# Optimization experiments

Hardware: AMD Instinct MI355X
Metric: run time of the kernel (lower is better)

The kernel has to match this reference:

```python
import jax, jax.numpy as jnp
import numpy as np

B, L, H, D, N, R, K = 1, 2048, 2048, 4096, 16, 128, 4


def setup_inputs() -> dict:
    key = jax.random.key(0)
    ks = jax.random.split(key, 10)
    s = 0.02
    x = jax.random.normal(ks[0], (B, L, H), dtype=jnp.float32)
    W_in = jax.random.normal(ks[1], (H, 2 * D), dtype=jnp.float32) * s
    conv_w = jax.random.normal(ks[2], (K, D), dtype=jnp.float32) * s  # depthwise causal conv
    conv_b = jnp.zeros((D,), dtype=jnp.float32)
    W_x = jax.random.normal(ks[3], (D, R + 2 * N), dtype=jnp.float32) * s
    W_dt = jax.random.normal(ks[4], (R, D), dtype=jnp.float32) * (R ** -0.5)
    # dt bias initialized so softplus(b_dt) ~ dt in [1e-3, 1e-1]
    dt = jnp.exp(jax.random.uniform(ks[5], (D,)) * (np.log(0.1) - np.log(1e-3)) + np.log(1e-3))
    b_dt = dt + jnp.log(-jnp.expm1(-dt))
    A_log = jnp.broadcast_to(jnp.log(jnp.arange(1, N + 1, dtype=jnp.float32)), (D, N))
    D_param = jnp.ones((D,), dtype=jnp.float32)
    W_out = jax.random.normal(ks[6], (D, H), dtype=jnp.float32) * s
    return {"x": x, "W_in": W_in, "conv_w": conv_w, "conv_b": conv_b,
            "W_x": W_x, "W_dt": W_dt, "b_dt": b_dt, "A_log": A_log,
            "D_param": D_param, "W_out": W_out}


def _mamba_fwd(x, W_in, conv_w, conv_b, W_x, W_dt, b_dt, A_log, D_param, W_out):
    silu = jax.nn.silu
    # in_proj then chunk into hidden / gate: [B,L,D] each
    proj = x @ W_in
    hs, gate = jnp.split(proj, 2, axis=-1)
    # causal depthwise conv along sequence (pad K-1 on the left)
    hs_pad = jnp.pad(hs, ((0, 0), (K - 1, 0), (0, 0)))
    conv = sum(hs_pad[:, k:k + L, :] * conv_w[k] for k in range(K)) + conv_b
    hs = silu(conv)  # [B,L,D]
    # ssm parameters
    ssm_p = hs @ W_x  # [B,L,R+2N]
    dt_in, Bm, Cm = jnp.split(ssm_p, [R, R + N], axis=-1)
    dt = jax.nn.softplus(dt_in @ W_dt + b_dt)  # [B,L,D]
    A = -jnp.exp(A_log)  # [D,N]
    dA = jnp.exp(dt[..., None] * A)                       # [B,L,D,N]
    dBu = dt[..., None] * Bm[:, :, None, :] * hs[..., None]  # [B,L,D,N]

    def step(s, inp):
        dA_t, dBu_t, C_t = inp
        s = dA_t * s + dBu_t                 # [B,D,N]
        y = jnp.einsum('bdn,bn->bd', s, C_t)
        return s, y

    s0 = jnp.zeros((B, D, N), dtype=x.dtype)
    xs = (jnp.moveaxis(dA, 1, 0), jnp.moveaxis(dBu, 1, 0), jnp.moveaxis(Cm, 1, 0))
    _, ys = jax.lax.scan(step, s0, xs)       # [L,B,D]
    y = jnp.moveaxis(ys, 0, 1)               # [B,L,D]
    y = y + hs * D_param
    y = y * silu(gate)
    return y @ W_out                          # [B,L,H]


def reference(x, W_in, conv_w, conv_b, W_x, W_dt, b_dt, A_log, D_param, W_out):
    return _mamba_fwd(x, W_in, conv_w, conv_b, W_x, W_dt, b_dt, A_log, D_param, W_out)
```

## Files before the change

### kernel.cpp

```cpp
#include <hip/hip_runtime.h>
#include <hip/hip_bf16.h>

typedef short short8 __attribute__((ext_vector_type(8)));
typedef float floatx4 __attribute__((ext_vector_type(4)));
using bf16 = __hip_bfloat16;

static constexpr int L = 2048, H = 2048, D = 4096, NS = 16, R = 128, KC = 4;
static constexpr int CCH = 64, TCH = L / CCH;
static constexpr int KSP = 16, KCHUNK = 4096 / KSP;
static constexpr int ZOUT = 4, KOUT = 4096 / ZOUT;

__device__ __forceinline__ void g2lds16(const void* g, void* l) {
  __builtin_amdgcn_global_load_lds((const __attribute__((address_space(1))) unsigned int*)g,
                                   (__attribute__((address_space(3))) unsigned int*)l,
                                   16, 0, 0);
}

__global__ void cast_f2b(const float* __restrict__ in, bf16* __restrict__ out, int n) {
  int i = blockIdx.x * 256 + threadIdx.x;
  if (i < n) out[i] = __float2bfloat16(in[i]);
}

__global__ void transpose_cast(const float* __restrict__ in, bf16* __restrict__ out,
                               int Rr, int Cc) {
  __shared__ float tile[32][33];
  int c0 = blockIdx.x * 32, r0 = blockIdx.y * 32;
  int tx = threadIdx.x, ty = threadIdx.y;
#pragma unroll
  for (int i = 0; i < 32; i += 8)
    tile[ty + i][tx] = in[(size_t)(r0 + ty + i) * Cc + (c0 + tx)];
  __syncthreads();
#pragma unroll
  for (int i = 0; i < 32; i += 8)
    out[(size_t)(c0 + ty + i) * Rr + (r0 + tx)] = __float2bfloat16(tile[tx][ty + i]);
}

template <int MODE>
__global__ __launch_bounds__(512, 2) void gemm256(
    const bf16* __restrict__ A, int lda,
    const bf16* __restrict__ Bt, int ldb,
    bf16* __restrict__ Cb, bf16* __restrict__ Cb2, int ldc, int K) {
  __shared__ short As[4 * 8192];
  __shared__ short Bs[4 * 8192];

  const int gx = gridDim.x;
  const int nwg = gx * gridDim.y;
  int id = blockIdx.y * gx + blockIdx.x;
  id = (id & 7) * (nwg >> 3) + (id >> 3);
  const int n0 = (id % gx) * 256;
  const int m0 = (id / gx) * 256;
  const int kbeg = (MODE == 3) ? blockIdx.z * K : 0;
  const int NT = K >> 6;

  const int tid = threadIdx.x;
  const int lane = tid & 63;
  const int w = tid >> 6;
  const int wm2 = w >> 2, wn4 = w & 3;
  const int lr = lane & 15, kq = lane >> 4;
  const int swzr = ((lane >> 3) & 1) << 1;
  const int ardo = (wm2 * 128 + lr) * 32 + (kq ^ swzr) * 8;
  const int brdo = (wn4 * 64 + lr) * 32 + (kq ^ swzr) * 8;
  const int srow = w * 16 + (lane >> 2);
  const int swzs = ((lane >> 5) & 1) << 1;
  const int scol = ((lane & 3) ^ swzs) * 8;

  floatx4 acc[8][4];
#pragma unroll
  for (int i = 0; i < 8; i++)
#pragma unroll
    for (int j = 0; j < 4; j++)
#pragma unroll
      for (int r = 0; r < 4; r++) acc[i][j][r] = 0.f;

  auto stageA = [&](short* pan, int kc) {
    const bf16* g = A + (size_t)(m0 + srow) * lda + (kbeg + kc + scol);
    g2lds16(g, pan + w * 512);
    g2lds16(g + (size_t)128 * lda, pan + 4096 + w * 512);
  };
  auto stageB = [&](short* pan, int kc) {
    const bf16* g = Bt + (size_t)(n0 + srow) * ldb + (kbeg + kc + scol);
    g2lds16(g, pan + w * 512);
    g2lds16(g + (size_t)128 * ldb, pan + 4096 + w * 512);
  };

#define LDA4(pan, base)                                               \
  _Pragma("unroll") for (int ii = 0; ii < 4; ii++)                    \
      af[ii] = *(const short8*)((pan) + ardo + ((base) + ii) * 512);
#define LDB4(pan)                                                     \
  _Pragma("unroll") for (int jj = 0; jj < 4; jj++)                    \
      bfr[jj] = *(const short8*)((pan) + brdo + jj * 512);
#define MFMA4(base)                                                   \
  _Pragma("unroll") for (int ii = 0; ii < 4; ii++)                    \
      _Pragma("unroll") for (int jj = 0; jj < 4; jj++)                \
          acc[(base) + ii][jj] = __builtin_amdgcn_mfma_f32_16x16x32_bf16( \
              af[ii], bfr[jj], acc[(base) + ii][jj], 0, 0, 0);
#define PHASE_SYNC()                                                  \
  __builtin_amdgcn_s_barrier();                                       \
  asm volatile("s_waitcnt lgkmcnt(0)" ::: "memory");                  \
  __builtin_amdgcn_sched_barrier(0);

  stageA(As + 0 * 8192, 0);
  stageB(Bs + 0 * 8192, 0);
  stageA(As + 1 * 8192, 32);
  stageB(Bs + 1 * 8192, 32);
  stageA(As + 2 * 8192, 64);
  stageB(Bs + 2 * 8192, 64);
  asm volatile("s_waitcnt vmcnt(4)" ::: "memory");
  __builtin_amdgcn_s_barrier();

#define GTILE(t, par)                                                      \
  {                                                                        \
    short* Ak0 = As + (par) * 16384;                                       \
    short* Bk0 = Bs + (par) * 16384;                                       \
    short* Ak1 = Ak0 + 8192;                                               \
    short* Bk1 = Bk0 + 8192;                                               \
    short* An1 = As + (1 - (par)) * 16384 + 8192;                          \
    short* Bn1 = Bs + (1 - (par)) * 16384 + 8192;                          \
    short8 af[4], bfr[4];                                                  \
                                           \
    LDA4(Ak0, 0); LDB4(Bk0);                                               \
    if ((t) + 1 < NT) stageA(An1, ((t) + 1) * 64 + 32);                    \
    PHASE_SYNC();                                                          \
    __builtin_amdgcn_s_setprio(1); MFMA4(0); __builtin_amdgcn_s_setprio(0);\
    __builtin_amdgcn_s_barrier();                                          \
                                           \
    LDA4(Ak0, 4);                                                          \
    if ((t) + 1 < NT) stageB(Bn1, ((t) + 1) * 64 + 32);                    \
    PHASE_SYNC();                                                          \
    __builtin_amdgcn_s_setprio(1); MFMA4(4); __builtin_amdgcn_s_setprio(0);\
    __builtin_amdgcn_s_barrier();                                          \
                                           \
    LDA4(Ak1, 0); LDB4(Bk1);                                               \
    if ((t) + 2 < NT) stageA(Ak0, ((t) + 2) * 64);                         \
    PHASE_SYNC();                                                          \
    __builtin_amdgcn_s_setprio(1); MFMA4(0); __builtin_amdgcn_s_setprio(0);\
    __builtin_amdgcn_s_barrier();                                          \
                                           \
    LDA4(Ak1, 4);                                                          \
    if ((t) + 2 < NT) stageB(Bk0, ((t) + 2) * 64);                         \
    PHASE_SYNC();                                                          \
    __builtin_amdgcn_s_setprio(1); MFMA4(4); __builtin_amdgcn_s_setprio(0);\
    __builtin_amdgcn_sched_barrier(0);                                     \
    if ((t) < NT - 2) {                                                    \
      asm volatile("s_waitcnt vmcnt(4)" ::: "memory");                     \
    } else {                                                               \
      asm volatile("s_waitcnt vmcnt(0)" ::: "memory");                     \
    }                                                                      \
    __builtin_amdgcn_sched_barrier(0);                                     \
    __builtin_amdgcn_s_barrier();                                          \
  }

  for (int t = 0; t < NT; t += 2) {
    GTILE(t, 0);
    GTILE(t + 1, 1);
  }
#undef GTILE
#undef PHASE_SYNC
#undef MFMA4
#undef LDB4
#undef LDA4

  bf16* base = Cb;
  int coff = 0, ld = ldc;
  if (MODE == 2) {
    if (n0 >= D) { base = Cb2; coff = D; }
    ld = D;
  }
  if (MODE == 3) base = Cb + (size_t)blockIdx.z * L * ldc;
  const int rb = kq * 4;
#pragma unroll
  for (int i = 0; i < 8; i++)
#pragma unroll
    for (int j = 0; j < 4; j++) {
      int col = n0 + wn4 * 64 + j * 16 + lr - coff;
      int row = m0 + wm2 * 128 + i * 16 + rb;
#pragma unroll
      for (int r = 0; r < 4; r++)
        base[(size_t)(row + r) * ld + col] = __float2bfloat16(acc[i][j][r]);
    }
}

template <int MODE>
__global__ __launch_bounds__(256) void gemm_async(
    const bf16* __restrict__ A, int lda,
    const bf16* __restrict__ Bt, int ldb,
    bf16* __restrict__ Cb, bf16* __restrict__ Cb2, int ldc, int K) {
  __shared__ short As[2 * 128 * 32];
  __shared__ short Bs[2 * 128 * 32];
  const int m0 = blockIdx.y * 128, n0 = blockIdx.x * 128;
  const int kbeg = (MODE == 3) ? blockIdx.z * K : 0;
  const int tid = threadIdx.x;
  const int lane = tid & 63;
  const int wave = tid >> 6;
  const int wm = (wave >> 1) * 64, wn = (wave & 1) * 64;
  const int lr = lane & 15, kq = lane >> 4;
  const int sr = lane >> 2, sc = (lane & 3) * 8;

  const bf16* Ab = A + (size_t)(m0 + wave * 16 + sr) * lda + sc;
  const bf16* Bb = Bt + (size_t)(n0 + wave * 16 + sr) * ldb + sc;
  short* Asw = &As[wave * 16 * 32];
  short* Bsw = &Bs[wave * 16 * 32];

  floatx4 acc[4][4];
#pragma unroll
  for (int i = 0; i < 4; i++)
#pragma unroll
    for (int j = 0; j < 4; j++)
#pragma unroll
      for (int r = 0; r < 4; r++) acc[i][j][r] = 0.f;

  for (int k0 = kbeg; k0 < kbeg + K; k0 += 64) {
    __syncthreads();
#pragma unroll
    for (int h = 0; h < 2; h++) {
      int kk = k0 + h * 32;
#pragma unroll
      for (int j = 0; j < 2; j++) {
        g2lds16(Ab + (size_t)j * 64 * lda + kk, Asw + h * 4096 + j * 64 * 32);
        g2lds16(Bb + (size_t)j * 64 * ldb + kk, Bsw + h * 4096 + j * 64 * 32);
      }
    }
    __syncthreads();
#pragma unroll
    for (int h = 0; h < 2; h++) {
      short8 af[4], bfr[4];
#pragma unroll
      for (int i = 0; i < 4; i++)
        af[i] = *(const short8*)(&As[h * 4096 + (wm + i * 16 + lr) * 32 + kq * 8]);
#pragma unroll
      for (int j = 0; j < 4; j++)
        bfr[j] = *(const short8*)(&Bs[h * 4096 + (wn + j * 16 + lr) * 32 + kq * 8]);
#pragma unroll
      for (int i = 0; i < 4; i++)
#pragma unroll
        for (int j = 0; j < 4; j++)
          acc[i][j] = __builtin_amdgcn_mfma_f32_16x16x32_bf16(af[i], bfr[j], acc[i][j], 0, 0, 0);
    }
  }

  bf16* base = Cb;
  int coff = 0, ld = ldc;
  if (MODE == 2) {
    if (n0 >= D) { base = Cb2; coff = D; }
    ld = D;
  }
  if (MODE == 3) base = Cb + (size_t)blockIdx.z * L * ldc;
  const int rb = kq * 4;
#pragma unroll
  for (int i = 0; i < 4; i++)
#pragma unroll
    for (int j = 0; j < 4; j++) {
      int col = n0 + wn + j * 16 + lr - coff;
      int row = m0 + wm + i * 16 + rb;
#pragma unroll
      for (int r = 0; r < 4; r++)
        base[(size_t)(row + r) * ld + col] = __float2bfloat16(acc[i][j][r]);
    }
}

__global__ void out_reduce(const unsigned short* __restrict__ P, float* __restrict__ out) {
  int i = blockIdx.x * 256 + threadIdx.x;
  const size_t LH = (size_t)L * H;
  float acc[8];
#pragma unroll
  for (int e = 0; e < 8; e++) acc[e] = 0.f;
#pragma unroll
  for (int z = 0; z < ZOUT; z++) {
    short8 v = *(const short8*)(P + z * LH + (size_t)i * 8);
#pragma unroll
    for (int e = 0; e < 8; e++)
      acc[e] += __uint_as_float(((unsigned)(unsigned short)v[e]) << 16);
  }
#pragma unroll
  for (int q = 0; q < 2; q++) {
    floatx4 o;
#pragma unroll
    for (int r = 0; r < 4; r++) o[r] = acc[q * 4 + r];
    *(floatx4*)(out + (size_t)i * 8 + q * 4) = o;
  }
}

__global__ __launch_bounds__(256) void gemm_splitk(
    const bf16* __restrict__ A, int lda,
    const bf16* __restrict__ Bt, int ldb,
    float* __restrict__ P, int ldc, int N) {
  __shared__ short As[128 * 40];
  __shared__ short Bs[128 * 40];
  const int m0 = blockIdx.y * 128, n0 = blockIdx.x * 128;
  const int kbeg = blockIdx.z * KCHUNK;
  float* C = P + (size_t)blockIdx.z * L * ldc;
  const int tid = threadIdx.x;
  const int lane = tid & 63;
  const int wave = tid >> 6;
  const int wm = (wave >> 1) * 64, wn = (wave & 1) * 64;
  const int lr = lane & 15, kq = lane >> 4;
  const int srow = tid >> 2, scol = (tid & 3) * 8;

  floatx4 acc[4][4];
#pragma unroll
  for (int i = 0; i < 4; i++)
#pragma unroll
    for (int j = 0; j < 4; j++)
#pragma unroll
      for (int r = 0; r < 4; r++) acc[i][j][r] = 0.f;

  for (int k0 = kbeg; k0 < kbeg + KCHUNK; k0 += 32) {
    __syncthreads();
#pragma unroll
    for (int h = 0; h < 2; h++) {
      int r = srow + h * 64;
      short8 va = *(const short8*)((const short*)A + (size_t)(m0 + r) * lda + k0 + scol);
      *(short8*)(&As[r * 40 + scol]) = va;
    }
#pragma unroll
    for (int h = 0; h < 2; h++) {
      int r = srow + h * 64;
      short8 vb;
      if ((n0 + r) < N) {
        vb = *(const short8*)((const short*)Bt + (size_t)(n0 + r) * ldb + k0 + scol);
      } else {
#pragma unroll
        for (int q = 0; q < 8; q++) vb[q] = 0;
      }
      *(short8*)(&Bs[r * 40 + scol]) = vb;
    }
    __syncthreads();
    short8 af[4], bfr[4];
#pragma unroll
    for (int i = 0; i < 4; i++)
      af[i] = *(const short8*)(&As[(wm + i * 16 + lr) * 40 + kq * 8]);
#pragma unroll
    for (int j = 0; j < 4; j++)
      bfr[j] = *(const short8*)(&Bs[(wn + j * 16 + lr) * 40 + kq * 8]);
#pragma unroll
    for (int i = 0; i < 4; i++)
#pragma unroll
      for (int j = 0; j < 4; j++)
        acc[i][j] = __builtin_amdgcn_mfma_f32_16x16x32_bf16(af[i], bfr[j], acc[i][j], 0, 0, 0);
  }

  const int rb = kq * 4;
#pragma unroll
  for (int i = 0; i < 4; i++)
#pragma unroll
    for (int j = 0; j < 4; j++) {
      int col = n0 + wn + j * 16 + lr;
      if (col >= N) continue;
      int row = m0 + wm + i * 16 + rb;
#pragma unroll
      for (int r = 0; r < 4; r++)
        C[(size_t)(row + r) * ldc + col] = acc[i][j][r];
    }
}

__global__ void splitk_reduce(const float* __restrict__ P, float* __restrict__ ssmp,
                              bf16* __restrict__ dtin) {
  int idx = blockIdx.x * 256 + threadIdx.x;
  float s = 0.f;
#pragma unroll
  for (int z = 0; z < KSP; z++) s += P[(size_t)z * L * 160 + idx];
  ssmp[idx] = s;
  int t = idx / 160, c = idx - t * 160;
  if (c < R) dtin[t * R + c] = __float2bfloat16(s);
}

__global__ void conv_silu(const bf16* __restrict__ projh,
                          const float* __restrict__ conv_w, const float* __restrict__ conv_b,
                          bf16* __restrict__ hs_b) {
  int idx = blockIdx.x * 256 + threadIdx.x;
  int d = idx & (D - 1), t = idx >> 12;
  float acc = conv_b[d];
#pragma unroll
  for (int k = 0; k < KC; k++) {
    int tt = t + k - (KC - 1);
    if (tt >= 0) acc += __bfloat162float(projh[(size_t)tt * D + d]) * conv_w[k * D + d];
  }
  float s = acc / (1.f + __expf(-acc));
  hs_b[idx] = __float2bfloat16(s);
}

__device__ __forceinline__ float softplusf(float v) {
  return (v > 20.f) ? v : log1pf(__expf(v));
}

__global__ __launch_bounds__(256) void scan_phase1(
    const bf16* __restrict__ dtraw, const float* __restrict__ b_dt,
    const bf16* __restrict__ hs_b, const float* __restrict__ ssmp,
    const float* __restrict__ A_log,
    float* __restrict__ sdt_out, float* __restrict__ S_out) {
  const int d = blockIdx.x * 256 + threadIdx.x;
  const int c = blockIdx.y;
  float An[NS];
#pragma unroll
  for (int n = 0; n < NS; n++) An[n] = -__expf(A_log[d * NS + n]);
  const float bdt = b_dt[d];
  float s[NS];
#pragma unroll
  for (int n = 0; n < NS; n++) s[n] = 0.f;
  float sdt = 0.f;
  const int t0 = c * TCH;
#pragma unroll 2
  for (int t = t0; t < t0 + TCH; t++) {
    float dtv = softplusf(__bfloat162float(dtraw[(size_t)t * D + d]) + bdt);
    float hsv = __bfloat162float(hs_b[(size_t)t * D + d]);
    sdt += dtv;
    float u = dtv * hsv;
    const float* Bp = ssmp + (size_t)t * 160 + 128;
#pragma unroll
    for (int n = 0; n < NS; n++) {
      float dA = __expf(An[n] * dtv);
      s[n] = dA * s[n] + Bp[n] * u;
    }
  }
  sdt_out[(size_t)c * D + d] = sdt;
  float* Sp = S_out + ((size_t)c * D + d) * NS;
#pragma unroll
  for (int n = 0; n < NS; n += 4)
    *(floatx4*)(Sp + n) = *(floatx4*)(s + n);
}

__global__ __launch_bounds__(256) void scan_phase2(
    const float* __restrict__ sdt, const float* __restrict__ S,
    const float* __restrict__ A_log, float* __restrict__ I) {
  int g = blockIdx.x * 256 + threadIdx.x;
  int d = g >> 4;
  float An = -__expf(A_log[g]);
  float cur = 0.f;
  float sdt_n = sdt[d];
  float S_n = S[g];
  for (int c = 0; c < CCH; c++) {
    float sdt_c = sdt_n, S_c = S_n;
    if (c + 1 < CCH) {
      sdt_n = sdt[(size_t)(c + 1) * D + d];
      S_n = S[(size_t)(c + 1) * D * NS + g];
    }
    I[(size_t)c * D * NS + g] = cur;
    cur = __expf(An * sdt_c) * cur + S_c;
  }
}

__global__ __launch_bounds__(256) void scan_phase3(
    const bf16* __restrict__ dtraw, const float* __restrict__ b_dt,
    const bf16* __restrict__ hs_b, const float* __restrict__ ssmp,
    const bf16* __restrict__ gate_b, const float* __restrict__ A_log,
    const float* __restrict__ D_param, const float* __restrict__ I,
    bf16* __restrict__ y_b) {
  const int d = blockIdx.x * 256 + threadIdx.x;
  const int c = blockIdx.y;
  float An[NS];
#pragma unroll
  for (int n = 0; n < NS; n++) An[n] = -__expf(A_log[d * NS + n]);
  const float bdt = b_dt[d];
  const float Dp = D_param[d];
  float s[NS];
  const float* Ip = I + ((size_t)c * D + d) * NS;
#pragma unroll
  for (int n = 0; n < NS; n += 4)
    *(floatx4*)(s + n) = *(const floatx4*)(Ip + n);
  const int t0 = c * TCH;
#pragma unroll 2
  for (int t = t0; t < t0 + TCH; t++) {
    float dtv = softplusf(__bfloat162float(dtraw[(size_t)t * D + d]) + bdt);
    float hsv = __bfloat162float(hs_b[(size_t)t * D + d]);
    float u = dtv * hsv;
    const float* Bp = ssmp + (size_t)t * 160 + 128;
    const float* Cp = ssmp + (size_t)t * 160 + 144;
    float y = 0.f;
#pragma unroll
    for (int n = 0; n < NS; n++) {
      float dA = __expf(An[n] * dtv);
      s[n] = dA * s[n] + Bp[n] * u;
      y += s[n] * Cp[n];
    }
    float gv = __bfloat162float(gate_b[(size_t)t * D + d]);
    float yv = (y + hsv * Dp) * (gv / (1.f + __expf(-gv)));
    y_b[(size_t)t * D + d] = __float2bfloat16(yv);
  }
}

extern "C" void kernel_launch(void* const* d_in, const int* in_sizes, int n_in,
                              void* d_out, int out_size, void* d_ws, size_t ws_size,
                              hipStream_t stream) {
  const float* x      = (const float*)d_in[0];
  const float* W_in   = (const float*)d_in[1];
  const float* conv_w = (const float*)d_in[2];
  const float* conv_b = (const float*)d_in[3];
  const float* W_x    = (const float*)d_in[4];
  const float* W_dt   = (const float*)d_in[5];
  const float* b_dt   = (const float*)d_in[6];
  const float* A_log  = (const float*)d_in[7];
  const float* D_par  = (const float*)d_in[8];
  const float* W_out  = (const float*)d_in[9];
  float* outp = (float*)d_out;

  char* ws = (char*)d_ws;
  size_t off = 0;
  auto alloc = [&](size_t bytes) {
    char* p = ws + off;
    off += (bytes + 255) & ~(size_t)255;
    return (void*)p;
  };
  bf16*  gate_b  = (bf16*) alloc((size_t)L * D * 2);
  bf16*  hs_b    = (bf16*) alloc((size_t)L * D * 2);
  float* ssmp    = (float*)alloc((size_t)L * 160 * 4);
  bf16*  dtin_b  = (bf16*) alloc((size_t)L * R * 2);
  bf16*  dtbuf_b = (bf16*) alloc((size_t)L * D * 2);
  bf16*  y_b     = (bf16*) alloc((size_t)L * D * 2);
  bf16*  WoutT   = (bf16*) alloc((size_t)H * D * 2);
  float* sdt     = (float*)alloc((size_t)CCH * D * 4);
  float* Sbuf    = (float*)alloc((size_t)CCH * D * NS * 4);
  float* Ibuf    = (float*)alloc((size_t)CCH * D * NS * 4);
  size_t tbase = off;
  bf16*  x_b     = (bf16*) alloc((size_t)L * H * 2);
  bf16*  WinT    = (bf16*) alloc((size_t)2 * D * H * 2);
  bf16*  WxT     = (bf16*) alloc((size_t)160 * D * 2);
  bf16*  WdtT    = (bf16*) alloc((size_t)D * R * 2);
  bf16*  projh_b = (bf16*) alloc((size_t)L * D * 2);
  float* part    = (float*)alloc((size_t)KSP * L * 160 * 4);
  bf16*  part2   = (bf16*)(ws + tbase);

  cast_f2b<<<(L * H) / 256, 256, 0, stream>>>(x, x_b, L * H);

  dim3 tb(32, 8);
  transpose_cast<<<dim3((2 * D) / 32, H / 32), tb, 0, stream>>>(W_in, WinT, H, 2 * D);
  transpose_cast<<<dim3(H / 32, D / 32), tb, 0, stream>>>(W_out, WoutT, D, H);
  transpose_cast<<<dim3(160 / 32, D / 32), tb, 0, stream>>>(W_x, WxT, D, 160);
  transpose_cast<<<dim3(D / 32, R / 32), tb, 0, stream>>>(W_dt, WdtT, R, D);

  gemm256<2><<<dim3((2 * D) / 256, L / 256), 512, 0, stream>>>(
      x_b, H, WinT, H, projh_b, gate_b, D, H);
  conv_silu<<<(L * D) / 256, 256, 0, stream>>>(projh_b, conv_w, conv_b, hs_b);
  gemm_splitk<<<dim3(2, L / 128, KSP), 256, 0, stream>>>(
      hs_b, D, WxT, D, part, 160, 160);
  splitk_reduce<<<(L * 160) / 256, 256, 0, stream>>>(part, ssmp, dtin_b);
  gemm_async<1><<<dim3(D / 128, L / 128), 256, 0, stream>>>(
      dtin_b, R, WdtT, R, dtbuf_b, nullptr, D, R);

  scan_phase1<<<dim3(D / 256, CCH), 256, 0, stream>>>(
      dtbuf_b, b_dt, hs_b, ssmp, A_log, sdt, Sbuf);
  scan_phase2<<<(D * NS) / 256, 256, 0, stream>>>(sdt, Sbuf, A_log, Ibuf);
  scan_phase3<<<dim3(D / 256, CCH), 256, 0, stream>>>(
      dtbuf_b, b_dt, hs_b, ssmp, gate_b, A_log, D_par, Ibuf, y_b);

  gemm256<3><<<dim3(H / 256, L / 256, ZOUT), 512, 0, stream>>>(
      y_b, D, WoutT, D, part2, nullptr, H, KOUT);
  out_reduce<<<(L * H) / (256 * 8), 256, 0, stream>>>((const unsigned short*)part2, outp);
}
```

Baseline: 476.3 us.

## Remap GEMM tiles per XCD and relax vmcnt waits for deeper prefetch

```diff
diff --git a/kernel.cpp b/kernel.cpp
--- a/kernel.cpp
+++ b/kernel.cpp
@@ -43,12 +43,14 @@
   __shared__ short As[4 * 8192];
   __shared__ short Bs[4 * 8192];
 
-  const int gx = gridDim.x;
-  const int nwg = gx * gridDim.y;
-  int id = blockIdx.y * gx + blockIdx.x;
-  id = (id & 7) * (nwg >> 3) + (id >> 3);
-  const int n0 = (id % gx) * 256;
-  const int m0 = (id / gx) * 256;
+  const int gx = gridDim.x, gy = gridDim.y;
+  const int orig = blockIdx.y * gx + blockIdx.x;
+  const int xcd = orig & 7;
+  const int rr = orig >> 3;
+  const int rn = gx >> 2, rm = gy >> 1;
+  const int tn = (xcd & 3) * rn + (rr % rn);
+  const int tm = (xcd >> 2) * rm + (rr / rn);
+  const int n0 = tn * 256, m0 = tm * 256;
   const int kbeg = (MODE == 3) ? blockIdx.z * K : 0;
   const int NT = K >> 6;
 
@@ -98,6 +100,10 @@
   __builtin_amdgcn_s_barrier();                                       \
   asm volatile("s_waitcnt lgkmcnt(0)" ::: "memory");                  \
   __builtin_amdgcn_sched_barrier(0);
+#define VMW(n)                                                        \
+  __builtin_amdgcn_sched_barrier(0);                                  \
+  asm volatile("s_waitcnt vmcnt(" #n ")" ::: "memory");               \
+  __builtin_amdgcn_sched_barrier(0);
 
   stageA(As + 0 * 8192, 0);
   stageB(Bs + 0 * 8192, 0);
@@ -105,7 +111,7 @@
   stageB(Bs + 1 * 8192, 32);
   stageA(As + 2 * 8192, 64);
   stageB(Bs + 2 * 8192, 64);
-  asm volatile("s_waitcnt vmcnt(4)" ::: "memory");
+  VMW(8);
   __builtin_amdgcn_s_barrier();
 
 #define GTILE(t, par)                                                      \
@@ -128,6 +134,7 @@
     if ((t) + 1 < NT) stageB(Bn1, ((t) + 1) * 64 + 32);                    \
     PHASE_SYNC();                                                          \
     __builtin_amdgcn_s_setprio(1); MFMA4(4); __builtin_amdgcn_s_setprio(0);\
+    if ((t) < NT - 1) { VMW(8); } else { VMW(0); }      \
     __builtin_amdgcn_s_barrier();                                          \
                                            \
     LDA4(Ak1, 0); LDB4(Bk1);                                               \
@@ -140,13 +147,10 @@
     if ((t) + 2 < NT) stageB(Bk0, ((t) + 2) * 64);                         \
     PHASE_SYNC();                                                          \
     __builtin_amdgcn_s_setprio(1); MFMA4(4); __builtin_amdgcn_s_setprio(0);\
-    __builtin_amdgcn_sched_barrier(0);                                     \
-    if ((t) < NT - 2) {                                                    \
-      asm volatile("s_waitcnt vmcnt(4)" ::: "memory");                     \
-    } else {                                                               \
-      asm volatile("s_waitcnt vmcnt(0)" ::: "memory");                     \
-    }                                                                      \
-    __builtin_amdgcn_sched_barrier(0);                                     \
+                                                      \
+    if ((t) < NT - 2) { VMW(8); }                                          \
+    else if ((t) == NT - 2) { VMW(4); }                                    \
+    else { VMW(0); }                                                       \
     __builtin_amdgcn_s_barrier();                                          \
   }
 
@@ -155,6 +159,7 @@
     GTILE(t + 1, 1);
   }
 #undef GTILE
+#undef VMW
 #undef PHASE_SYNC
 #undef MFMA4
 #undef LDB4
```

Result: no change. 478.5 us (+0.5%).
